# Optimization experiments

Measured on AMD Instinct MI355X. Metric: run time of the kernel, lower is better.

Reference implementation:

```python
import jax, jax.numpy as jnp
import numpy as np

B, T, CNN, HW = 512, 256, 512, 7
V, H = 37, 8  # vocab_size, hidden_size


def setup_inputs() -> dict:
    key = jax.random.key(0)
    ks = jax.random.split(key, 10)
    s = 0.1
    return {
        "features": jax.random.normal(ks[0], (B, CNN, HW, HW), jnp.float32),
        "captions": jax.random.normal(ks[1], (B, T, V), jnp.float32),
        "W_in": jax.random.normal(ks[2], (V, CNN), jnp.float32) * s,
        "b_in": jax.random.normal(ks[3], (V,), jnp.float32) * s,
        "W_ih": jax.random.normal(ks[4], (4 * H, V), jnp.float32) * s,
        "W_hh": jax.random.normal(ks[5], (4 * H, H), jnp.float32) * s,
        "b_ih": jax.random.normal(ks[6], (4 * H,), jnp.float32) * s,
        "b_hh": jax.random.normal(ks[7], (4 * H,), jnp.float32) * s,
        "W_out": jax.random.normal(ks[8], (V, H), jnp.float32) * s,
        "b_out": jax.random.normal(ks[9], (V,), jnp.float32) * s,
    }


def reference(features, captions, W_in, b_in, W_ih, W_hh, b_ih, b_hh, W_out, b_out):
    # AdaptiveAvgPool2d(1) + flatten + fc_in -> [B, V]
    feat = features.mean(axis=(2, 3)) @ W_in.T + b_in
    # input at t=0 is feat, at t>0 is captions[:, t-1]; build [T, B, V] sequence
    xs = jnp.concatenate([feat[None], jnp.swapaxes(captions, 0, 1)[:-1]], axis=0)

    def step(carry, x):
        h, c = carry
        gates = x @ W_ih.T + b_ih + h @ W_hh.T + b_hh  # [B, 4H]
        i, f, g, o = jnp.split(gates, 4, axis=1)  # PyTorch LSTMCell gate order
        i = jax.nn.sigmoid(i)
        f = jax.nn.sigmoid(f)
        g = jnp.tanh(g)
        o = jax.nn.sigmoid(o)
        c = f * c + i * g
        h = o * jnp.tanh(c)
        out = jax.nn.softmax(h @ W_out.T + b_out, axis=1)  # [B, V]
        return (h, c), out

    h0 = jnp.zeros((feat.shape[0], W_hh.shape[1]), feat.dtype)
    c0 = jnp.zeros_like(h0)
    _, outs = jax.lax.scan(step, (h0, c0), xs)  # outs: [T, B, V]
    return jnp.swapaxes(outs, 0, 1)  # [B, T, V]
```

## Files before the change

kernel.cpp:

```cpp
#include <hip/hip_runtime.h>
#include <math.h>

#define BB   512
#define TT   256
#define CNNC 512
#define VV   37
#define HH   8
#define G4   32
#define CH   32
#define CW   (CH * 128)

#define L2E 1.4426950408889634f

typedef float f4_t __attribute__((ext_vector_type(4)));

__device__ __forceinline__ void async_copy16(const float* g, float* l) {
    __builtin_amdgcn_global_load_lds(
        (__attribute__((address_space(1))) void*)g,
        (__attribute__((address_space(3))) void*)l, 16, 0, 0);
}

template <int CTRL>
__device__ __forceinline__ float dpp_f(float x) {
    int r = __builtin_amdgcn_update_dpp(0, __float_as_int(x), CTRL, 0xF, 0xF, true);
    return __int_as_float(r);
}

__device__ __forceinline__ float rcp_f(float x) { return __builtin_amdgcn_rcpf(x); }
__device__ __forceinline__ float exp2_f(float x) { return __builtin_amdgcn_exp2f(x); }

__global__ __launch_bounds__(256) void k_feat(const float* __restrict__ features,
                                              const float* __restrict__ W_in,
                                              const float* __restrict__ b_in,
                                              float* __restrict__ featp) {
    __shared__ __align__(16) float raw[128 * 49];
    __shared__ float pooled[128];
    const int b = blockIdx.x, qt = blockIdx.y, tid = threadIdx.x;
    const f4_t* src =
        (const f4_t*)(features + (size_t)b * CNNC * 49 + qt * (128 * 49));
    f4_t* dst = (f4_t*)raw;
    for (int i = tid; i < 128 * 49 / 4; i += 256)
        dst[i] = __builtin_nontemporal_load(&src[i]);
    __syncthreads();
    if (tid < 128) {
        const float* p = raw + tid * 49;
        float s = 0.f;
        #pragma unroll
        for (int i = 0; i < 49; ++i) s += p[i];
        pooled[tid] = s;
    }
    __syncthreads();
    const int v = tid >> 2, pp = tid & 3;
    if (v < VV) {
        const float* w = W_in + v * CNNC + qt * 128 + pp * 32;
        const float* q = pooled + pp * 32;
        float s = 0.f;
        #pragma unroll
        for (int i = 0; i < 32; ++i) s += q[i] * w[i];
        s += __shfl_xor(s, 1);
        s += __shfl_xor(s, 2);
        if (pp == 0)
            featp[(qt * BB + b) * VV + v] =
                s * (1.f / 49.f) + (qt == 0 ? b_in[v] : 0.f);
    }
}

#define CAPS 1188
#define SOS  132
__global__ __launch_bounds__(256) void k_xproj(const float* __restrict__ captions,
                                               const float* __restrict__ W_ih,
                                               const float* __restrict__ b_ih,
                                               const float* __restrict__ b_hh,
                                               const float* __restrict__ featp,
                                               float* __restrict__ xproj) {
    __shared__ float W[G4 * VV];
    __shared__ float bias[G4];
    __shared__ float cap[4 * CAPS];
    __shared__ __align__(16) float so[32 * SOS];
    const int bg = blockIdx.x, tile = blockIdx.y;
    const int tid = threadIdx.x;
    for (int i = tid; i < G4 * VV; i += 256) W[i] = W_ih[i];
    if (tid < G4) bias[tid] = b_ih[tid] + b_hh[tid];

    const int t0 = tile * 32;
    const int start = (tile == 0) ? 0 : t0 - 1;
    for (int i = tid; i < 4 * 1184; i += 256) {
        const int s2 = i / 1184;
        const int off = i - s2 * 1184;
        cap[s2 * CAPS + off] = __builtin_nontemporal_load(
            &captions[((size_t)(bg * 4 + s2) * TT + start) * VV + off]);
    }
    __syncthreads();

    const int tl = tid >> 3;
    const int s  = (tid >> 1) & 3;
    const int r  = tid & 1;
    const int t  = t0 + tl;
    const int b  = bg * 4 + s;

    float xr[VV];
    if (tile == 0 && tl == 0) {
        #pragma unroll
        for (int v = 0; v < VV; ++v)
            xr[v] = featp[b * VV + v] + featp[(BB + b) * VV + v] +
                    featp[(2 * BB + b) * VV + v] + featp[(3 * BB + b) * VV + v];
    } else {
        const int lr = (tile == 0) ? tl - 1 : tl;
        const float* x = &cap[s * CAPS + lr * VV];
        #pragma unroll
        for (int v = 0; v < VV; ++v) xr[v] = x[v];
    }

    const int g0 = r * 16;
    float acc[16];
    #pragma unroll
    for (int g = 0; g < 16; ++g) acc[g] = bias[g0 + g];
    #pragma unroll
    for (int v = 0; v < VV; ++v) {
        const float xv = xr[v];
        #pragma unroll
        for (int g = 0; g < 16; ++g) acc[g] += xv * W[(g0 + g) * VV + v];
    }
    #pragma unroll
    for (int g = 0; g < 16; ++g) {
        const int gg = g0 + g;
        const float sc = (gg >= 16 && gg < 24) ? (-2.f * L2E) : (-L2E);
        so[tl * SOS + gg * 4 + s] = acc[g] * sc;
    }
    __syncthreads();

    float* chunk = xproj + ((size_t)bg * TT + t0) * 128;
    for (int i = tid; i < 1024; i += 256) {
        const int t2 = i >> 5, rest = i & 31;
        f4_t val = *(const f4_t*)&so[t2 * SOS + rest * 4];
        *(f4_t*)&chunk[t2 * 128 + rest * 4] = val;
    }
}

__global__ __launch_bounds__(64) void k_lstm(const float* __restrict__ W_hh,
                                             const float* __restrict__ xproj,
                                             float* __restrict__ hbuf) {
    __shared__ __align__(16) float buf[3 * CW + 128];
    const int lane = threadIdx.x;
    const int s4 = lane >> 4;
    const int q  = lane & 15;
    const int j  = q >> 1;
    const int r  = q & 1;

    const int rowA = r * 8 + j;
    const int rowB = 16 + r * 8 + j;
    const float scA = -L2E;
    const float scB = r ? -L2E : (-2.f * L2E);
    float wA[HH], wB[HH];
    #pragma unroll
    for (int m = 0; m < HH; ++m) {
        wA[m] = scA * W_hh[rowA * HH + (j ^ m)];
        wB[m] = scB * W_hh[rowB * HH + (j ^ m)];
    }

    const int bg = blockIdx.x;
    const float* xp = xproj + (size_t)bg * (TT * 128);
    float* hb = hbuf + ((size_t)(bg * 4 + s4) * TT) * HH + j;
    const int roff = rowA * 4 + s4;

    #pragma unroll
    for (int it = 0; it < 16; ++it)
        async_copy16(xp + (it * 64 + lane) * 4, &buf[it * 256]);
    #pragma unroll
    for (int it = 0; it < 16; ++it)
        async_copy16(xp + CW + (it * 64 + lane) * 4, &buf[CW + it * 256]);

    float h = 0.f, c = 0.f;
    for (int ck = 0; ck < TT / CH; ++ck) {
        if (ck == 0)      asm volatile("s_waitcnt vmcnt(16)" ::: "memory");
        else if (ck == 7) asm volatile("s_waitcnt vmcnt(32)" ::: "memory");
        else              asm volatile("s_waitcnt vmcnt(48)" ::: "memory");

        const float* base = &buf[(ck % 3) * CW] + roff;
        float hsv[CH];
        float pA = base[0], pB = base[64];
        #pragma unroll
        for (int tl = 0; tl < CH; ++tl) {
            const float nA = base[(tl + 1) * 128];
            const float nB = base[(tl + 1) * 128 + 64];

            const float ha0 = h;
            const float ha1 = dpp_f<0x4E>(h);
            const float ha3 = dpp_f<0x141>(h);
            const float ha2 = dpp_f<0x4E>(ha3);
            const float ha7 = dpp_f<0x140>(h);
            const float ha4 = dpp_f<0x141>(ha7);
            const float ha5 = dpp_f<0x4E>(ha4);
            const float ha6 = dpp_f<0x1B>(ha7);

            float a0 = fmaf(wA[0], ha0, pA);
            a0 = fmaf(wA[1], ha1, a0);
            a0 = fmaf(wA[2], ha2, a0);
            a0 = fmaf(wA[3], ha3, a0);
            float a1 = wA[4] * ha4;
            a1 = fmaf(wA[5], ha5, a1);
            a1 = fmaf(wA[6], ha6, a1);
            a1 = fmaf(wA[7], ha7, a1);
            const float npA = a0 + a1;
            float b0 = fmaf(wB[0], ha0, pB);
            b0 = fmaf(wB[1], ha1, b0);
            b0 = fmaf(wB[2], ha2, b0);
            b0 = fmaf(wB[3], ha3, b0);
            float b1 = wB[4] * ha4;
            b1 = fmaf(wB[5], ha5, b1);
            b1 = fmaf(wB[6], ha6, b1);
            b1 = fmaf(wB[7], ha7, b1);
            const float npB = b0 + b1;

            const float eA = rcp_f(1.f + exp2_f(npA));
            const float uB = rcp_f(1.f + exp2_f(npB));
            const float gg = fmaf(2.f, uB, -1.f);

            const float myU = r ? eA : eA * gg;
            const float otU = dpp_f<0xB1>(myU);
            const float fg  = r ? myU : otU;
            const float igg = r ? otU : myU;
            const float ogx = dpp_f<0xB1>(uB);
            const float og  = r ? uB : ogx;

            c = fmaf(fg, c, igg);
            const float th =
                fmaf(2.f, rcp_f(1.f + exp2_f(c * (-2.f * L2E))), -1.f);
            h = og * th;
            hsv[tl] = h;
            pA = nA; pB = nB;
        }
        if (r == 0) {
            #pragma unroll
            for (int i = 0; i < CH; ++i) hb[(ck * CH + i) * HH] = hsv[i];
        }
        if (ck + 2 < TT / CH) {
            const float* src = xp + (size_t)(ck + 2) * CW;
            float* db = &buf[((ck + 2) % 3) * CW];
            #pragma unroll
            for (int it = 0; it < 16; ++it)
                async_copy16(src + (it * 64 + lane) * 4, &db[it * 256]);
        }
    }
}

__global__ __launch_bounds__(128) void k_out(const float* __restrict__ hbuf,
                                             const float* __restrict__ W_out,
                                             const float* __restrict__ b_out,
                                             float* __restrict__ out) {
    __shared__ float W[VV * HH];
    __shared__ float bo[VV];
    __shared__ __align__(16) float stage[128 * VV];
    const int b = blockIdx.x, half = blockIdx.y, tid = threadIdx.x;
    for (int i = tid; i < VV * HH; i += 128) W[i] = W_out[i];
    if (tid < VV) bo[tid] = b_out[tid];
    __syncthreads();

    const int t = half * 128 + tid;
    const f4_t* hp = (const f4_t*)(hbuf + ((size_t)b * TT + t) * HH);
    const f4_t h0 = hp[0], h1 = hp[1];
    const float hr[HH] = {h0.x, h0.y, h0.z, h0.w, h1.x, h1.y, h1.z, h1.w};

    float z[VV];
    float m = -1e30f;
    #pragma unroll
    for (int v = 0; v < VV; ++v) {
        float sv = bo[v];
        #pragma unroll
        for (int k = 0; k < HH; ++k) sv += hr[k] * W[v * HH + k];
        z[v] = sv;
        m = fmaxf(m, sv);
    }
    float sum = 0.f;
    #pragma unroll
    for (int v = 0; v < VV; ++v) {
        z[v] = exp2_f((z[v] - m) * L2E);
        sum += z[v];
    }
    const float rs = rcp_f(sum);
    #pragma unroll
    for (int v = 0; v < VV; ++v) stage[tid * VV + v] = z[v] * rs;
    __syncthreads();

    f4_t* ob = (f4_t*)(out + ((size_t)b * TT + half * 128) * VV);
    const f4_t* sg = (const f4_t*)stage;
    for (int i = tid; i < 128 * VV / 4; i += 128)
        __builtin_nontemporal_store(sg[i], &ob[i]);
}

extern "C" void kernel_launch(void* const* d_in, const int* in_sizes, int n_in,
                              void* d_out, int out_size, void* d_ws, size_t ws_size,
                              hipStream_t stream) {
    const float* features = (const float*)d_in[0];
    const float* captions = (const float*)d_in[1];
    const float* W_in     = (const float*)d_in[2];
    const float* b_in     = (const float*)d_in[3];
    const float* W_ih     = (const float*)d_in[4];
    const float* W_hh     = (const float*)d_in[5];
    const float* b_ih     = (const float*)d_in[6];
    const float* b_hh     = (const float*)d_in[7];
    const float* W_out    = (const float*)d_in[8];
    const float* b_out    = (const float*)d_in[9];
    float* out = (float*)d_out;

    float* ws    = (float*)d_ws;
    float* featp = ws;
    float* xproj = ws + 81920;
    float* hbuf  = ws + 81920 + 4194304;

    k_feat <<<dim3(BB, 4),  256, 0, stream>>>(features, W_in, b_in, featp);
    k_xproj<<<dim3(128, 8), 256, 0, stream>>>(captions, W_ih, b_ih, b_hh, featp, xproj);
    k_lstm <<<128,           64, 0, stream>>>(W_hh, xproj, hbuf);
    k_out  <<<dim3(BB, 2),  128, 0, stream>>>(hbuf, W_out, b_out, out);
}
```

Measured before the change: 196.2 us.

## Fuse input projection, LSTM recurrence and output softmax into one warp-specialized kernel

Replaces the separate xproj, LSTM and output kernels with one 256-thread block per 4-sequence group. One wave runs the recurrence, two waves compute the gate projections for the next 32-step chunk, and one wave computes softmax outputs for the previous chunk and stages captions, all double-buffered in LDS. This removes the global round trips for xproj and the hidden states and two kernel launches. In exchange, the serial recurrence wave now waits at a block barrier every chunk, and the producer waves read weights directly from global memory.

New measurement: 382.0 us. 94.7% more time.

```diff
diff --git a/kernel.cpp b/kernel.cpp
--- a/kernel.cpp
+++ b/kernel.cpp
@@ -8,24 +8,17 @@
 #define HH   8
 #define G4   32
 #define CH   32
-#define CW   (CH * 128)
+#define NCK  8
 
 #define L2E 1.4426950408889634f
 
 typedef float f4_t __attribute__((ext_vector_type(4)));
-
-__device__ __forceinline__ void async_copy16(const float* g, float* l) {
-    __builtin_amdgcn_global_load_lds(
-        (__attribute__((address_space(1))) void*)g,
-        (__attribute__((address_space(3))) void*)l, 16, 0, 0);
-}
 
 template <int CTRL>
 __device__ __forceinline__ float dpp_f(float x) {
     int r = __builtin_amdgcn_update_dpp(0, __float_as_int(x), CTRL, 0xF, 0xF, true);
     return __int_as_float(r);
 }
-
 __device__ __forceinline__ float rcp_f(float x) { return __builtin_amdgcn_rcpf(x); }
 __device__ __forceinline__ float exp2_f(float x) { return __builtin_amdgcn_exp2f(x); }
 
@@ -65,227 +58,232 @@
     }
 }
 
-#define CAPS 1188
-#define SOS  132
-__global__ __launch_bounds__(256) void k_xproj(const float* __restrict__ captions,
-                                               const float* __restrict__ W_ih,
-                                               const float* __restrict__ b_ih,
-                                               const float* __restrict__ b_hh,
-                                               const float* __restrict__ featp,
-                                               float* __restrict__ xproj) {
-    __shared__ float W[G4 * VV];
-    __shared__ float bias[G4];
-    __shared__ float cap[4 * CAPS];
-    __shared__ __align__(16) float so[32 * SOS];
-    const int bg = blockIdx.x, tile = blockIdx.y;
-    const int tid = threadIdx.x;
-    for (int i = tid; i < G4 * VV; i += 256) W[i] = W_ih[i];
-    if (tid < G4) bias[tid] = b_ih[tid] + b_hh[tid];
-
-    const int t0 = tile * 32;
-    const int start = (tile == 0) ? 0 : t0 - 1;
-    for (int i = tid; i < 4 * 1184; i += 256) {
-        const int s2 = i / 1184;
-        const int off = i - s2 * 1184;
-        cap[s2 * CAPS + off] = __builtin_nontemporal_load(
-            &captions[((size_t)(bg * 4 + s2) * TT + start) * VV + off]);
-    }
-    __syncthreads();
-
-    const int tl = tid >> 3;
-    const int s  = (tid >> 1) & 3;
-    const int r  = tid & 1;
-    const int t  = t0 + tl;
-    const int b  = bg * 4 + s;
-
-    float xr[VV];
-    if (tile == 0 && tl == 0) {
+#define XSTR 133
+#define XBUF 4400
+#define CSEQ 1280
+#define OSTR 1188
+
+__device__ __forceinline__ void stage_chunk(float* __restrict__ cap,
+                                            const float* __restrict__ captions,
+                                            int b0, int buf, int cc,
+                                            int lane, int nthreads) {
+    float* cb = cap + buf * (4 * CSEQ);
+    if (cc == 0) {
+        for (int i = lane; i < 4 * 1147; i += nthreads) {
+            const int s = i / 1147, o = i - s * 1147;
+            const int row = o / 37, v = o - row * 37;
+            cb[s * CSEQ + (row + 1) * 40 + v] = __builtin_nontemporal_load(
+                &captions[(size_t)(b0 + s) * TT * VV + o]);
+        }
+    } else {
+        const int src0 = (cc * 32 - 1) * 37;
+        for (int i = lane; i < 4 * 1184; i += nthreads) {
+            const int s = i / 1184, o = i - s * 1184;
+            const int row = o / 37, v = o - row * 37;
+            cb[s * CSEQ + row * 40 + v] = __builtin_nontemporal_load(
+                &captions[(size_t)(b0 + s) * TT * VV + src0 + o]);
+        }
+    }
+}
+
+__device__ __forceinline__ void produce_chunk(float* __restrict__ xb,
+                                              const float* __restrict__ cap_s,
+                                              const float* __restrict__ W_ih,
+                                              const float* __restrict__ b_ih,
+                                              const float* __restrict__ b_hh,
+                                              const float* __restrict__ featp,
+                                              int b0, int cc, int lt, int s) {
+    float xr[40];
+    if (cc == 0 && lt == 0) {
+        const int b = b0 + s;
         #pragma unroll
         for (int v = 0; v < VV; ++v)
             xr[v] = featp[b * VV + v] + featp[(BB + b) * VV + v] +
                     featp[(2 * BB + b) * VV + v] + featp[(3 * BB + b) * VV + v];
     } else {
-        const int lr = (tile == 0) ? tl - 1 : tl;
-        const float* x = &cap[s * CAPS + lr * VV];
-        #pragma unroll
-        for (int v = 0; v < VV; ++v) xr[v] = x[v];
-    }
-
-    const int g0 = r * 16;
-    float acc[16];
+        const f4_t* xp4 = (const f4_t*)(cap_s + s * CSEQ + lt * 40);
+        #pragma unroll
+        for (int v4 = 0; v4 < 10; ++v4) {
+            const f4_t x4 = xp4[v4];
+            xr[v4 * 4 + 0] = x4.x; xr[v4 * 4 + 1] = x4.y;
+            xr[v4 * 4 + 2] = x4.z; xr[v4 * 4 + 3] = x4.w;
+        }
+    }
+    float* od = xb + lt * XSTR + s;
     #pragma unroll
-    for (int g = 0; g < 16; ++g) acc[g] = bias[g0 + g];
+    for (int g = 0; g < G4; ++g) {
+        float acc = b_ih[g] + b_hh[g];
+        #pragma unroll
+        for (int v = 0; v < VV; ++v) acc = fmaf(W_ih[g * VV + v], xr[v], acc);
+        const float sc = (g >= 16 && g < 24) ? (-2.f * L2E) : (-L2E);
+        od[g * 4] = acc * sc;
+    }
+}
+
+__device__ __forceinline__ void consume_chunk(const float* __restrict__ hl,
+                                              float* __restrict__ ostage,
+                                              const float* __restrict__ W_out,
+                                              const float* __restrict__ b_out,
+                                              float* __restrict__ out,
+                                              int b0, int cc, int wl) {
     #pragma unroll
-    for (int v = 0; v < VV; ++v) {
-        const float xv = xr[v];
-        #pragma unroll
-        for (int g = 0; g < 16; ++g) acc[g] += xv * W[(g0 + g) * VV + v];
-    }
-    #pragma unroll
-    for (int g = 0; g < 16; ++g) {
-        const int gg = g0 + g;
-        const float sc = (gg >= 16 && gg < 24) ? (-2.f * L2E) : (-L2E);
-        so[tl * SOS + gg * 4 + s] = acc[g] * sc;
-    }
+    for (int k = 0; k < 2; ++k) {
+        const int rid = wl + 64 * k;
+        const int s = rid >> 5, lt = rid & 31;
+        const f4_t* hp = (const f4_t*)(hl + (lt * 4 + s) * 8);
+        const f4_t h0 = hp[0], h1 = hp[1];
+        const float hr[8] = {h0.x, h0.y, h0.z, h0.w, h1.x, h1.y, h1.z, h1.w};
+        float z[VV], m = -1e30f;
+        #pragma unroll
+        for (int v = 0; v < VV; ++v) {
+            float sv = b_out[v];
+            #pragma unroll
+            for (int kk = 0; kk < 8; ++kk)
+                sv = fmaf(hr[kk], W_out[v * 8 + kk], sv);
+            z[v] = sv; m = fmaxf(m, sv);
+        }
+        float sum = 0.f;
+        #pragma unroll
+        for (int v = 0; v < VV; ++v) { z[v] = exp2_f((z[v] - m) * L2E); sum += z[v]; }
+        const float rs = rcp_f(sum);
+        #pragma unroll
+        for (int v = 0; v < VV; ++v) ostage[s * OSTR + lt * 37 + v] = z[v] * rs;
+    }
+    asm volatile("s_waitcnt lgkmcnt(0)" ::: "memory");
+    for (int i = wl; i < 4 * 296; i += 64) {
+        const int s = i / 296, o = i - s * 296;
+        const f4_t val = *(const f4_t*)&ostage[s * OSTR + o * 4];
+        f4_t* dst = (f4_t*)(out + ((size_t)(b0 + s) * TT + cc * 32) * VV) + o;
+        __builtin_nontemporal_store(val, dst);
+    }
+}
+
+__global__ __launch_bounds__(256) void k_fused(const float* __restrict__ captions,
+                                               const float* __restrict__ W_ih,
+                                               const float* __restrict__ b_ih,
+                                               const float* __restrict__ b_hh,
+                                               const float* __restrict__ W_hh,
+                                               const float* __restrict__ W_out,
+                                               const float* __restrict__ b_out,
+                                               const float* __restrict__ featp,
+                                               float* __restrict__ out) {
+    __shared__ __align__(16) float cap[2 * 4 * CSEQ];
+    __shared__ __align__(16) float xbuf[2 * XBUF];
+    __shared__ __align__(16) float hlds[2 * 1024];
+    __shared__ __align__(16) float ostage[4 * OSTR];
+
+    const int tid = threadIdx.x;
+    const int wid = tid >> 6, wl = tid & 63;
+    const int bg = blockIdx.x, b0 = bg * 4;
+
+    float wA[HH] = {0}, wB[HH] = {0};
+    int s4 = 0, j = 0, r = 0, roff = 0;
+    if (wid == 0) {
+        s4 = wl >> 4;
+        const int q = wl & 15;
+        j = q >> 1; r = q & 1;
+        const int rowA = r * 8 + j, rowB = 16 + r * 8 + j;
+        const float scA = -L2E, scB = r ? -L2E : (-2.f * L2E);
+        #pragma unroll
+        for (int m = 0; m < HH; ++m) {
+            wA[m] = scA * W_hh[rowA * HH + (j ^ m)];
+            wB[m] = scB * W_hh[rowB * HH + (j ^ m)];
+        }
+        roff = rowA * 4 + s4;
+    }
+
+    stage_chunk(cap, captions, b0, 0, 0, tid, 256);
+    stage_chunk(cap, captions, b0, 1, 1, tid, 256);
     __syncthreads();
-
-    float* chunk = xproj + ((size_t)bg * TT + t0) * 128;
-    for (int i = tid; i < 1024; i += 256) {
-        const int t2 = i >> 5, rest = i & 31;
-        f4_t val = *(const f4_t*)&so[t2 * SOS + rest * 4];
-        *(f4_t*)&chunk[t2 * 128 + rest * 4] = val;
-    }
-}
-
-__global__ __launch_bounds__(64) void k_lstm(const float* __restrict__ W_hh,
-                                             const float* __restrict__ xproj,
-                                             float* __restrict__ hbuf) {
-    __shared__ __align__(16) float buf[3 * CW + 128];
-    const int lane = threadIdx.x;
-    const int s4 = lane >> 4;
-    const int q  = lane & 15;
-    const int j  = q >> 1;
-    const int r  = q & 1;
-
-    const int rowA = r * 8 + j;
-    const int rowB = 16 + r * 8 + j;
-    const float scA = -L2E;
-    const float scB = r ? -L2E : (-2.f * L2E);
-    float wA[HH], wB[HH];
-    #pragma unroll
-    for (int m = 0; m < HH; ++m) {
-        wA[m] = scA * W_hh[rowA * HH + (j ^ m)];
-        wB[m] = scB * W_hh[rowB * HH + (j ^ m)];
-    }
-
-    const int bg = blockIdx.x;
-    const float* xp = xproj + (size_t)bg * (TT * 128);
-    float* hb = hbuf + ((size_t)(bg * 4 + s4) * TT) * HH + j;
-    const int roff = rowA * 4 + s4;
-
-    #pragma unroll
-    for (int it = 0; it < 16; ++it)
-        async_copy16(xp + (it * 64 + lane) * 4, &buf[it * 256]);
-    #pragma unroll
-    for (int it = 0; it < 16; ++it)
-        async_copy16(xp + CW + (it * 64 + lane) * 4, &buf[CW + it * 256]);
+    if (wid == 1 || wid == 2) {
+        const int p = (wid - 1) * 64 + wl;
+        produce_chunk(&xbuf[0], &cap[0], W_ih, b_ih, b_hh, featp,
+                      b0, 0, p & 31, p >> 5);
+    }
+    __syncthreads();
 
     float h = 0.f, c = 0.f;
-    for (int ck = 0; ck < TT / CH; ++ck) {
-        if (ck == 0)      asm volatile("s_waitcnt vmcnt(16)" ::: "memory");
-        else if (ck == 7) asm volatile("s_waitcnt vmcnt(32)" ::: "memory");
-        else              asm volatile("s_waitcnt vmcnt(48)" ::: "memory");
-
-        const float* base = &buf[(ck % 3) * CW] + roff;
-        float hsv[CH];
-        float pA = base[0], pB = base[64];
-        #pragma unroll
-        for (int tl = 0; tl < CH; ++tl) {
-            const float nA = base[(tl + 1) * 128];
-            const float nB = base[(tl + 1) * 128 + 64];
-
-            const float ha0 = h;
-            const float ha1 = dpp_f<0x4E>(h);
-            const float ha3 = dpp_f<0x141>(h);
-            const float ha2 = dpp_f<0x4E>(ha3);
-            const float ha7 = dpp_f<0x140>(h);
-            const float ha4 = dpp_f<0x141>(ha7);
-            const float ha5 = dpp_f<0x4E>(ha4);
-            const float ha6 = dpp_f<0x1B>(ha7);
-
-            float a0 = fmaf(wA[0], ha0, pA);
-            a0 = fmaf(wA[1], ha1, a0);
-            a0 = fmaf(wA[2], ha2, a0);
-            a0 = fmaf(wA[3], ha3, a0);
-            float a1 = wA[4] * ha4;
-            a1 = fmaf(wA[5], ha5, a1);
-            a1 = fmaf(wA[6], ha6, a1);
-            a1 = fmaf(wA[7], ha7, a1);
-            const float npA = a0 + a1;
-            float b0 = fmaf(wB[0], ha0, pB);
-            b0 = fmaf(wB[1], ha1, b0);
-            b0 = fmaf(wB[2], ha2, b0);
-            b0 = fmaf(wB[3], ha3, b0);
-            float b1 = wB[4] * ha4;
-            b1 = fmaf(wB[5], ha5, b1);
-            b1 = fmaf(wB[6], ha6, b1);
-            b1 = fmaf(wB[7], ha7, b1);
-            const float npB = b0 + b1;
-
-            const float eA = rcp_f(1.f + exp2_f(npA));
-            const float uB = rcp_f(1.f + exp2_f(npB));
-            const float gg = fmaf(2.f, uB, -1.f);
-
-            const float myU = r ? eA : eA * gg;
-            const float otU = dpp_f<0xB1>(myU);
-            const float fg  = r ? myU : otU;
-            const float igg = r ? otU : myU;
-            const float ogx = dpp_f<0xB1>(uB);
-            const float og  = r ? uB : ogx;
-
-            c = fmaf(fg, c, igg);
-            const float th =
-                fmaf(2.f, rcp_f(1.f + exp2_f(c * (-2.f * L2E))), -1.f);
-            h = og * th;
-            hsv[tl] = h;
-            pA = nA; pB = nB;
-        }
-        if (r == 0) {
-            #pragma unroll
-            for (int i = 0; i < CH; ++i) hb[(ck * CH + i) * HH] = hsv[i];
-        }
-        if (ck + 2 < TT / CH) {
-            const float* src = xp + (size_t)(ck + 2) * CW;
-            float* db = &buf[((ck + 2) % 3) * CW];
-            #pragma unroll
-            for (int it = 0; it < 16; ++it)
-                async_copy16(src + (it * 64 + lane) * 4, &db[it * 256]);
-        }
-    }
-}
-
-__global__ __launch_bounds__(128) void k_out(const float* __restrict__ hbuf,
-                                             const float* __restrict__ W_out,
-                                             const float* __restrict__ b_out,
-                                             float* __restrict__ out) {
-    __shared__ float W[VV * HH];
-    __shared__ float bo[VV];
-    __shared__ __align__(16) float stage[128 * VV];
-    const int b = blockIdx.x, half = blockIdx.y, tid = threadIdx.x;
-    for (int i = tid; i < VV * HH; i += 128) W[i] = W_out[i];
-    if (tid < VV) bo[tid] = b_out[tid];
-    __syncthreads();
-
-    const int t = half * 128 + tid;
-    const f4_t* hp = (const f4_t*)(hbuf + ((size_t)b * TT + t) * HH);
-    const f4_t h0 = hp[0], h1 = hp[1];
-    const float hr[HH] = {h0.x, h0.y, h0.z, h0.w, h1.x, h1.y, h1.z, h1.w};
-
-    float z[VV];
-    float m = -1e30f;
-    #pragma unroll
-    for (int v = 0; v < VV; ++v) {
-        float sv = bo[v];
-        #pragma unroll
-        for (int k = 0; k < HH; ++k) sv += hr[k] * W[v * HH + k];
-        z[v] = sv;
-        m = fmaxf(m, sv);
-    }
-    float sum = 0.f;
-    #pragma unroll
-    for (int v = 0; v < VV; ++v) {
-        z[v] = exp2_f((z[v] - m) * L2E);
-        sum += z[v];
-    }
-    const float rs = rcp_f(sum);
-    #pragma unroll
-    for (int v = 0; v < VV; ++v) stage[tid * VV + v] = z[v] * rs;
-    __syncthreads();
-
-    f4_t* ob = (f4_t*)(out + ((size_t)b * TT + half * 128) * VV);
-    const f4_t* sg = (const f4_t*)stage;
-    for (int i = tid; i < 128 * VV / 4; i += 128)
-        __builtin_nontemporal_store(sg[i], &ob[i]);
+    for (int ck = 0; ck <= NCK; ++ck) {
+        if (wid == 0) {
+            if (ck < NCK) {
+                const float* base = &xbuf[(ck & 1) * XBUF] + roff;
+                float* hl = &hlds[(ck & 1) * 1024];
+                float hsv[CH];
+                float pA = base[0], pB = base[64];
+                #pragma unroll 4
+                for (int tl = 0; tl < CH; ++tl) {
+                    const float nA = base[(tl + 1) * XSTR];
+                    const float nB = base[(tl + 1) * XSTR + 64];
+
+                    const float ha0 = h;
+                    const float ha1 = dpp_f<0x4E>(h);
+                    const float ha3 = dpp_f<0x141>(h);
+                    const float ha2 = dpp_f<0x4E>(ha3);
+                    const float ha7 = dpp_f<0x140>(h);
+                    const float ha4 = dpp_f<0x141>(ha7);
+                    const float ha5 = dpp_f<0x4E>(ha4);
+                    const float ha6 = dpp_f<0x1B>(ha7);
+
+                    float a0 = fmaf(wA[0], ha0, pA);
+                    a0 = fmaf(wA[1], ha1, a0);
+                    a0 = fmaf(wA[2], ha2, a0);
+                    a0 = fmaf(wA[3], ha3, a0);
+                    float a1 = wA[4] * ha4;
+                    a1 = fmaf(wA[5], ha5, a1);
+                    a1 = fmaf(wA[6], ha6, a1);
+                    a1 = fmaf(wA[7], ha7, a1);
+                    const float npA = a0 + a1;
+                    float b0f = fmaf(wB[0], ha0, pB);
+                    b0f = fmaf(wB[1], ha1, b0f);
+                    b0f = fmaf(wB[2], ha2, b0f);
+                    b0f = fmaf(wB[3], ha3, b0f);
+                    float b1f = wB[4] * ha4;
+                    b1f = fmaf(wB[5], ha5, b1f);
+                    b1f = fmaf(wB[6], ha6, b1f);
+                    b1f = fmaf(wB[7], ha7, b1f);
+                    const float npB = b0f + b1f;
+
+                    const float eA = rcp_f(1.f + exp2_f(npA));
+                    const float uB = rcp_f(1.f + exp2_f(npB));
+                    const float gg = fmaf(2.f, uB, -1.f);
+
+                    const float myU = r ? eA : eA * gg;
+                    const float otU = dpp_f<0xB1>(myU);
+                    const float fg  = r ? myU : otU;
+                    const float igg = r ? otU : myU;
+                    const float ogx = dpp_f<0xB1>(uB);
+                    const float og  = r ? uB : ogx;
+
+                    c = fmaf(fg, c, igg);
+                    const float th =
+                        fmaf(2.f, rcp_f(1.f + exp2_f(c * (-2.f * L2E))), -1.f);
+                    h = og * th;
+                    hsv[tl] = h;
+                    pA = nA; pB = nB;
+                }
+                if (r == 0) {
+                    #pragma unroll
+                    for (int i = 0; i < CH; ++i)
+                        hl[(i * 4 + s4) * 8 + j] = hsv[i];
+                }
+            }
+        } else if (wid <= 2) {
+            if (ck + 1 < NCK) {
+                const int p = (wid - 1) * 64 + wl;
+                produce_chunk(&xbuf[((ck + 1) & 1) * XBUF],
+                              &cap[((ck + 1) & 1) * (4 * CSEQ)],
+                              W_ih, b_ih, b_hh, featp, b0, ck + 1,
+                              p & 31, p >> 5);
+            }
+        } else {
+            if (ck >= 1)
+                consume_chunk(&hlds[((ck - 1) & 1) * 1024], ostage,
+                              W_out, b_out, out, b0, ck - 1, wl);
+            if (ck + 2 < NCK)
+                stage_chunk(cap, captions, b0, (ck + 2) & 1, ck + 2, wl, 64);
+        }
+        __syncthreads();
+    }
 }
 
 extern "C" void kernel_launch(void* const* d_in, const int* in_sizes, int n_in,
@@ -303,13 +301,9 @@
     const float* b_out    = (const float*)d_in[9];
     float* out = (float*)d_out;
 
-    float* ws    = (float*)d_ws;
-    float* featp = ws;
-    float* xproj = ws + 81920;
-    float* hbuf  = ws + 81920 + 4194304;
-
-    k_feat <<<dim3(BB, 4),  256, 0, stream>>>(features, W_in, b_in, featp);
-    k_xproj<<<dim3(128, 8), 256, 0, stream>>>(captions, W_ih, b_ih, b_hh, featp, xproj);
-    k_lstm <<<128,           64, 0, stream>>>(W_hh, xproj, hbuf);
-    k_out  <<<dim3(BB, 2),  128, 0, stream>>>(hbuf, W_out, b_out, out);
-}
+    float* featp = (float*)d_ws;
+
+    k_feat <<<dim3(BB, 4), 256, 0, stream>>>(features, W_in, b_in, featp);
+    k_fused<<<128,         256, 0, stream>>>(captions, W_ih, b_ih, b_hh, W_hh,
+                                             W_out, b_out, featp, out);
+}
```
